# Optimization experiments

Measured on AMD Instinct MI355X. Metric: run time of the kernel, lower is better.

The kernel has to match this reference:

```python
import jax, jax.numpy as jnp
import numpy as np

N_SAMPLES = 2 ** 15  # 32768
NYQUIST = 22050.0 / 2.0
MIN_FREQ = 40.0 / NYQUIST
MAX_FREQ = 4000.0 / NYQUIST
FREQ_RANGE = MAX_FREQ - MIN_FREQ


def interp_linear(x, out_size):
    """torch F.interpolate(mode='linear', align_corners=False) along last axis."""
    in_size = x.shape[-1]
    scale = in_size / out_size
    coords = (jnp.arange(out_size, dtype=x.dtype) + 0.5) * scale - 0.5
    coords = jnp.clip(coords, 0.0, in_size - 1)
    lo = jnp.floor(coords).astype(jnp.int32)
    hi = jnp.minimum(lo + 1, in_size - 1)
    w = coords - lo.astype(x.dtype)
    return x[..., lo] * (1.0 - w) + x[..., hi] * w


def translate(pair, shift, scale):
    # angle of complex(pair[:,:,0], pair[:,:,1]) / pi, then affine
    angle = jnp.arctan2(pair[:, :, 1, :], pair[:, :, 0, :]) / np.pi
    return shift + angle * scale


def setup_inputs() -> dict:
    key = jax.random.key(0)
    k1, k2 = jax.random.split(key)
    x = jax.random.normal(k1, (16, 8, 10, 128), dtype=jnp.float32)
    noise = jax.random.normal(k2, (16, 8, N_SAMPLES), dtype=jnp.float32)
    return {"x": x, "noise": noise}


def reference(x, noise):
    # x: (batch, n_osc, 10, time_ctrl); noise: (batch, n_osc, N_SAMPLES)
    basic = x[:, :, 0:2, :]
    amp = jnp.sqrt(jnp.sum(basic * basic, axis=2))            # (b, o, t)
    amp = interp_linear(amp, N_SAMPLES)                       # (b, o, N)

    f0 = translate(basic, MIN_FREQ, FREQ_RANGE)               # control-rate
    mix = interp_linear(translate(x[:, :, 2:4, :], 1.0, 0.5), N_SAMPLES)
    harm_amp = amp * mix
    noise_amp = amp * (1.0 - mix)

    noise_std = translate(x[:, :, 4:6, :], MIN_FREQ, FREQ_RANGE)
    mod_factor = translate(x[:, :, 6:8, :], 0.25, 4.75)
    b = translate(x[:, :, 8:10, :], 0.1, 9.9)

    # band_filtered_noise: narrowband noise as a frequency-jittered sine
    f0_fr = interp_linear(f0, N_SAMPLES)
    std_fr = interp_linear(noise_std, N_SAMPLES)
    bfn = jnp.sin(jnp.cumsum(f0_fr + noise * std_fr, axis=-1))
    noise_sig = noise_amp * bfn

    mod_factor = interp_linear(mod_factor, N_SAMPLES)
    b = interp_linear(b, N_SAMPLES)
    mod = b * jnp.sin(jnp.cumsum(mod_factor, axis=-1))
    sig = harm_amp * jnp.sin(jnp.cumsum(f0_fr, axis=-1) + mod)

    mixed = noise_sig + sig                                   # (b, o, N)
    return jnp.mean(mixed, axis=1, keepdims=True)             # (b, 1, N)
```

## Files before the change

### kernel.cpp

```cpp
#include <hip/hip_runtime.h>
#include <math.h>

#define NS     32768
#define NB     128
#define CELL   32
#define CPB    32
#define PART   (CELL * CPB)
#define NPARTS (NS / PART)
#define TPB    256
#define NBATCH 16
#define GRID   (NBATCH * NPARTS)
#define NBIN   6

__device__ __forceinline__ float sinr(float x) {
    return __builtin_amdgcn_sinf(x - rintf(x));
}

__device__ __forceinline__ void seg_params(int i, int& lo, int& hi,
                                           double& w0, double& wst) {
    if (i < 128)            { lo = 0;   hi = 1;   w0 = 0.0; wst = 0.0; }
    else if (i >= NS - 128) { lo = 127; hi = 127; w0 = 0.0; wst = 0.0; }
    else {
        lo = (i - 128) >> 8;  hi = lo + 1;
        int off = (i - 128) & 255;
        w0 = (off + 0.5) * (1.0 / 256.0);
        wst = 1.0 / 256.0;
    }
}

__device__ __forceinline__ double bin_value(const float* xs, int q, int j) {
    const double PI_    = 3.14159265358979323846;
    const double INV2PI = 0.15915494309189533576888376337251;
    const double MINF   = 40.0 / 11025.0;
    const double FRNG   = (4000.0 - 40.0) / 11025.0;
    if (q == 0) {
        double a0 = (double)xs[j], a1 = (double)xs[NB + j];
        return sqrt(a0 * a0 + a1 * a1);
    }
    double ang = atan2((double)xs[(2 * q - 1) * NB + j],
                       (double)xs[(2 * q - 2) * NB + j]) / PI_;
    double sh, sc;
    if      (q == 1) { sh = MINF; sc = FRNG; }
    else if (q == 2) { sh = 1.0;  sc = 0.5;  }
    else if (q == 3) { sh = MINF; sc = FRNG; }
    else if (q == 4) { sh = 0.25; sc = 4.75; }
    else             { sh = 0.1;  sc = 9.9;  }
    double v = sh + ang * sc;
    if (q != 2) v *= INV2PI;
    return v;
}

__device__ __forceinline__ void cell_totals(
        const float4* nn, double f0L, double dF0, double stL, double dSt,
        double mfL, double dMf, double w0, double wst,
        double& t1, double& t3, double& t2) {
    float s0 = 0.f, s1 = 0.f;
    #pragma unroll
    for (int q4 = 0; q4 < CELL / 4; ++q4) {
        float4 nv = nn[q4];
        float jd = (float)(q4 * 4);
        s0 += nv.x; s1 = fmaf(jd, nv.x, s1);
        s0 += nv.y; s1 = fmaf(jd + 1.f, nv.y, s1);
        s0 += nv.z; s1 = fmaf(jd + 2.f, nv.z, s1);
        s0 += nv.w; s1 = fmaf(jd + 3.f, nv.w, s1);
    }
    double S0 = (double)s0, S1 = (double)s1;
    double sw = 32.0 * w0 + 496.0 * wst;
    t3 = 32.0 * f0L + dF0 * sw;
    t2 = 32.0 * mfL + dMf * sw;
    t1 = t3 + stL * S0 + dSt * (w0 * S0 + wst * S1);
}

__global__ __launch_bounds__(TPB)
void span_kernel(const float* __restrict__ xg, const float* __restrict__ ng,
                 double* __restrict__ wspan) {
    __shared__ double binsA[8][3][NBIN];

    int bx = blockIdx.x, bb = bx >> 5, p = bx & (NPARTS - 1);
    int tid = threadIdx.x, lane = tid & 63;
    int h = tid >> 5, c = tid & 31;
    int P = p * PART;
    int b0 = (P - 128) >> 8; if (b0 < 0) b0 = 0;
    int s  = (bb << 3) + h;
    int i0 = P + c * CELL;

    if (tid < 144) {
        int j = tid % NBIN, r = (tid / NBIN) % 3, h2 = tid / (3 * NBIN);
        int q = (r == 0) ? 1 : (r == 1) ? 3 : 4;
        const float* xs = xg + (size_t)((bb << 3) + h2) * 10 * NB;
        binsA[h2][r][j] = bin_value(xs, q, min(b0 + j, NB - 1));
    }
    __syncthreads();

    int lo, hi; double w0, wst;
    seg_params(i0, lo, hi, w0, wst);
    int jL = lo - b0, jH = hi - b0;
    double f0L = binsA[h][0][jL], dF0 = binsA[h][0][jH] - f0L;
    double stL = binsA[h][1][jL], dSt = binsA[h][1][jH] - stL;
    double mfL = binsA[h][2][jL], dMf = binsA[h][2][jH] - mfL;

    const float4* nn = reinterpret_cast<const float4*>(ng + (size_t)s * NS + i0);
    double t1, t3, t2;
    cell_totals(nn, f0L, dF0, stL, dSt, mfL, dMf, w0, wst, t1, t3, t2);

    double v1 = t1, v3 = t3, v2 = t2;
    #pragma unroll
    for (int d = 1; d < 32; d <<= 1) {
        double u1 = __shfl_up(v1, d);
        double u3 = __shfl_up(v3, d);
        double u2 = __shfl_up(v2, d);
        if ((lane & 31) >= d) { v1 += u1; v3 += u3; v2 += u2; }
    }
    if (c == 31) {
        size_t sb = ((size_t)s * NPARTS + p) * 3;
        wspan[sb + 0] = v1; wspan[sb + 1] = v3; wspan[sb + 2] = v2;
    }
}

__global__ __launch_bounds__(TPB)
void fm_kernel(const float* __restrict__ xg, const float* __restrict__ ng,
               const double* __restrict__ wspan, float* __restrict__ out) {
    __shared__ double binsA[8][3][NBIN];
    __shared__ float  binsB[8][6][NBIN];
    __shared__ double wtot[4][8][3];
    __shared__ double prefL[8][3];

    int bx = blockIdx.x, bb = bx >> 5, p = bx & (NPARTS - 1);
    int tid = threadIdx.x, lane = tid & 63, wid = tid >> 6;
    int h = tid & 7, c = tid >> 3;
    int P = p * PART;
    int b0 = (P - 128) >> 8; if (b0 < 0) b0 = 0;
    int s  = (bb << 3) + h;
    int i0 = P + c * CELL;

    if (tid < 192) {
        int r = tid & 7, g = tid >> 3, k = g % 3, h2 = g / 3;
        const double* sp = wspan + ((size_t)(((bb << 3) + h2) * NPARTS)) * 3 + k;
        double acc = 0.0;
        #pragma unroll
        for (int q = 0; q < NPARTS / 8; ++q) {
            int idx = r + q * 8;
            if (idx < p) acc += sp[idx * 3];
        }
        #pragma unroll
        for (int m = 1; m <= 4; m <<= 1) acc += __shfl_xor(acc, m);
        if (r == 0) prefL[h2][k] = acc;
    }
    for (int idx = tid; idx < 8 * 6 * NBIN; idx += TPB) {
        int j = idx % NBIN, q = (idx / NBIN) % 6, h2 = idx / (6 * NBIN);
        const float* xs = xg + (size_t)((bb << 3) + h2) * 10 * NB;
        double v = bin_value(xs, q, min(b0 + j, NB - 1));
        binsB[h2][q][j] = (float)v;
        if      (q == 1) binsA[h2][0][j] = v;
        else if (q == 3) binsA[h2][1][j] = v;
        else if (q == 4) binsA[h2][2][j] = v;
    }
    __syncthreads();

    int lo, hi; double w0, wst;
    seg_params(i0, lo, hi, w0, wst);
    int jL = lo - b0, jH = hi - b0;
    double f0L = binsA[h][0][jL], dF0 = binsA[h][0][jH] - f0L;
    double stL = binsA[h][1][jL], dSt = binsA[h][1][jH] - stL;
    double mfL = binsA[h][2][jL], dMf = binsA[h][2][jH] - mfL;

    const float4* nn = reinterpret_cast<const float4*>(ng + (size_t)s * NS + i0);
    double t1, t3, t2;
    cell_totals(nn, f0L, dF0, stL, dSt, mfL, dMf, w0, wst, t1, t3, t2);

    double v1 = t1, v3 = t3, v2 = t2;
    #pragma unroll
    for (int d = 8; d < 64; d <<= 1) {
        double u1 = __shfl_up(v1, d);
        double u3 = __shfl_up(v3, d);
        double u2 = __shfl_up(v2, d);
        if (lane >= d) { v1 += u1; v3 += u3; v2 += u2; }
    }
    if (lane >= 56) { wtot[wid][h][0] = v1; wtot[wid][h][1] = v3; wtot[wid][h][2] = v2; }
    __syncthreads();
    double b1 = 0.0, b3 = 0.0, b2 = 0.0;
    #pragma unroll
    for (int k = 0; k < 3; ++k)
        if (wid > k) { b1 += wtot[k][h][0]; b3 += wtot[k][h][1]; b2 += wtot[k][h][2]; }

    double a1 = prefL[h][0] + b1 + (v1 - t1);
    double a3 = prefL[h][1] + b3 + (v3 - t3);
    double a2 = prefL[h][2] + b2 + (v2 - t2);
    float fr1 = (float)(a1 - rint(a1));
    float fr3 = (float)(a3 - rint(a3));
    float fr2 = (float)(a2 - rint(a2));

    float amL = binsB[h][0][jL], dAm = binsB[h][0][jH] - amL;
    float g0L = binsB[h][1][jL], gF0 = binsB[h][1][jH] - g0L;
    float mxL = binsB[h][2][jL], dMx = binsB[h][2][jH] - mxL;
    float gsL = binsB[h][3][jL], gSt = binsB[h][3][jH] - gsL;
    float gmL = binsB[h][4][jL], gMf = binsB[h][4][jH] - gmL;
    float bbL = binsB[h][5][jL], dBb = binsB[h][5][jH] - bbL;
    float w0f = (float)w0, wsf = (float)wst;

    float arr[CELL];
    float d1 = 0.f, d2 = 0.f, d3 = 0.f;
    #pragma unroll
    for (int q4 = 0; q4 < CELL / 4; ++q4) {
        float4 nv = nn[q4];
        float nf[4] = {nv.x, nv.y, nv.z, nv.w};
        #pragma unroll
        for (int u = 0; u < 4; ++u) {
            int j = q4 * 4 + u;
            float wf  = fmaf((float)j, wsf, w0f);
            float f0v = fmaf(wf, gF0, g0L);
            float stv = fmaf(wf, gSt, gsL);
            float mfv = fmaf(wf, gMf, gmL);
            d3 += f0v;
            d1 += fmaf(nf[u], stv, f0v);
            d2 += mfv;
            float ampv = fmaf(wf, dAm, amL);
            float mixv = fmaf(wf, dMx, mxL);
            float bv   = fmaf(wf, dBb, bbL);
            float s2 = sinr(fr2 + d2);
            float s1 = sinr(fr1 + d1);
            float s3 = sinr(fmaf(bv, s2, fr3 + d3));
            float harm = ampv * mixv;
            arr[j] = fmaf(harm, s3, (ampv - harm) * s1);
        }
    }

    #pragma unroll
    for (int m = 1; m <= 4; m <<= 1) {
        #pragma unroll
        for (int j = 0; j < CELL; ++j) arr[j] += __shfl_xor(arr[j], m);
    }
    if (h == 0) {
        float4* op = reinterpret_cast<float4*>(out + (size_t)bb * NS + i0);
        #pragma unroll
        for (int j4 = 0; j4 < CELL / 4; ++j4)
            op[j4] = make_float4(arr[j4 * 4 + 0] * 0.125f, arr[j4 * 4 + 1] * 0.125f,
                                 arr[j4 * 4 + 2] * 0.125f, arr[j4 * 4 + 3] * 0.125f);
    }
}

extern "C" void kernel_launch(void* const* d_in, const int* in_sizes, int n_in,
                              void* d_out, int out_size, void* d_ws, size_t ws_size,
                              hipStream_t stream) {
    const float* x     = (const float*)d_in[0];
    const float* noise = (const float*)d_in[1];
    float* out = (float*)d_out;
    double* wspan = (double*)d_ws;
    span_kernel<<<GRID, TPB, 0, stream>>>(x, noise, wspan);
    fm_kernel<<<GRID, TPB, 0, stream>>>(x, noise, wspan, out);
}
```

Before: 79.56 us.

## Fuse span and FM kernels into one cooperative launch with grid sync

Merges the two-pass scan (span partial sums, then FM synthesis) into a single cooperative kernel that writes per-part totals, does a grid-wide sync, then reads the prefix. Noise values are kept in registers across the sync, so noise is read once instead of twice. This removes a kernel launch and the redundant bin and noise work of the first pass. The cost is a grid barrier, a requirement that all 512 blocks be co-resident (launch bounds set to 2 blocks per CU), and extra register pressure; it falls back to the two-kernel path if the cooperative launch fails.

Result: slower. 140.5 us (+76.6%).

```diff
diff --git a/kernel.cpp b/kernel.cpp
--- a/kernel.cpp
+++ b/kernel.cpp
@@ -1,5 +1,8 @@
 #include <hip/hip_runtime.h>
+#include <hip/hip_cooperative_groups.h>
 #include <math.h>
+
+namespace cg = cooperative_groups;
 
 #define NS     32768
 #define NB     128
@@ -51,8 +54,8 @@
 }
 
 __device__ __forceinline__ void cell_totals(
-        const float4* nn, double f0L, double dF0, double stL, double dSt,
-        double mfL, double dMf, double w0, double wst,
+        const float4 (&nn)[CELL / 4], double f0L, double dF0, double stL,
+        double dSt, double mfL, double dMf, double w0, double wst,
         double& t1, double& t3, double& t2) {
     float s0 = 0.f, s1 = 0.f;
     #pragma unroll
@@ -71,55 +74,9 @@
     t1 = t3 + stL * S0 + dSt * (w0 * S0 + wst * S1);
 }
 
-__global__ __launch_bounds__(TPB)
-void span_kernel(const float* __restrict__ xg, const float* __restrict__ ng,
-                 double* __restrict__ wspan) {
-    __shared__ double binsA[8][3][NBIN];
-
-    int bx = blockIdx.x, bb = bx >> 5, p = bx & (NPARTS - 1);
-    int tid = threadIdx.x, lane = tid & 63;
-    int h = tid >> 5, c = tid & 31;
-    int P = p * PART;
-    int b0 = (P - 128) >> 8; if (b0 < 0) b0 = 0;
-    int s  = (bb << 3) + h;
-    int i0 = P + c * CELL;
-
-    if (tid < 144) {
-        int j = tid % NBIN, r = (tid / NBIN) % 3, h2 = tid / (3 * NBIN);
-        int q = (r == 0) ? 1 : (r == 1) ? 3 : 4;
-        const float* xs = xg + (size_t)((bb << 3) + h2) * 10 * NB;
-        binsA[h2][r][j] = bin_value(xs, q, min(b0 + j, NB - 1));
-    }
-    __syncthreads();
-
-    int lo, hi; double w0, wst;
-    seg_params(i0, lo, hi, w0, wst);
-    int jL = lo - b0, jH = hi - b0;
-    double f0L = binsA[h][0][jL], dF0 = binsA[h][0][jH] - f0L;
-    double stL = binsA[h][1][jL], dSt = binsA[h][1][jH] - stL;
-    double mfL = binsA[h][2][jL], dMf = binsA[h][2][jH] - mfL;
-
-    const float4* nn = reinterpret_cast<const float4*>(ng + (size_t)s * NS + i0);
-    double t1, t3, t2;
-    cell_totals(nn, f0L, dF0, stL, dSt, mfL, dMf, w0, wst, t1, t3, t2);
-
-    double v1 = t1, v3 = t3, v2 = t2;
-    #pragma unroll
-    for (int d = 1; d < 32; d <<= 1) {
-        double u1 = __shfl_up(v1, d);
-        double u3 = __shfl_up(v3, d);
-        double u2 = __shfl_up(v2, d);
-        if ((lane & 31) >= d) { v1 += u1; v3 += u3; v2 += u2; }
-    }
-    if (c == 31) {
-        size_t sb = ((size_t)s * NPARTS + p) * 3;
-        wspan[sb + 0] = v1; wspan[sb + 1] = v3; wspan[sb + 2] = v2;
-    }
-}
-
-__global__ __launch_bounds__(TPB)
-void fm_kernel(const float* __restrict__ xg, const float* __restrict__ ng,
-               const double* __restrict__ wspan, float* __restrict__ out) {
+__global__ __launch_bounds__(TPB, 2)
+void fused_kernel(const float* __restrict__ xg, const float* __restrict__ ng,
+                  double* __restrict__ wspan, float* __restrict__ out) {
     __shared__ double binsA[8][3][NBIN];
     __shared__ float  binsB[8][6][NBIN];
     __shared__ double wtot[4][8][3];
@@ -133,19 +90,6 @@
     int s  = (bb << 3) + h;
     int i0 = P + c * CELL;
 
-    if (tid < 192) {
-        int r = tid & 7, g = tid >> 3, k = g % 3, h2 = g / 3;
-        const double* sp = wspan + ((size_t)(((bb << 3) + h2) * NPARTS)) * 3 + k;
-        double acc = 0.0;
-        #pragma unroll
-        for (int q = 0; q < NPARTS / 8; ++q) {
-            int idx = r + q * 8;
-            if (idx < p) acc += sp[idx * 3];
-        }
-        #pragma unroll
-        for (int m = 1; m <= 4; m <<= 1) acc += __shfl_xor(acc, m);
-        if (r == 0) prefL[h2][k] = acc;
-    }
     for (int idx = tid; idx < 8 * 6 * NBIN; idx += TPB) {
         int j = idx % NBIN, q = (idx / NBIN) % 6, h2 = idx / (6 * NBIN);
         const float* xs = xg + (size_t)((bb << 3) + h2) * 10 * NB;
@@ -160,13 +104,19 @@
     int lo, hi; double w0, wst;
     seg_params(i0, lo, hi, w0, wst);
     int jL = lo - b0, jH = hi - b0;
-    double f0L = binsA[h][0][jL], dF0 = binsA[h][0][jH] - f0L;
-    double stL = binsA[h][1][jL], dSt = binsA[h][1][jH] - stL;
-    double mfL = binsA[h][2][jL], dMf = binsA[h][2][jH] - mfL;
-
-    const float4* nn = reinterpret_cast<const float4*>(ng + (size_t)s * NS + i0);
+
+    const float4* np_ = reinterpret_cast<const float4*>(ng + (size_t)s * NS + i0);
+    float4 nv[CELL / 4];
+    #pragma unroll
+    for (int q4 = 0; q4 < CELL / 4; ++q4) nv[q4] = np_[q4];
+
     double t1, t3, t2;
-    cell_totals(nn, f0L, dF0, stL, dSt, mfL, dMf, w0, wst, t1, t3, t2);
+    {
+        double f0L = binsA[h][0][jL], dF0 = binsA[h][0][jH] - f0L;
+        double stL = binsA[h][1][jL], dSt = binsA[h][1][jH] - stL;
+        double mfL = binsA[h][2][jL], dMf = binsA[h][2][jH] - mfL;
+        cell_totals(nv, f0L, dF0, stL, dSt, mfL, dMf, w0, wst, t1, t3, t2);
+    }
 
     double v1 = t1, v3 = t3, v2 = t2;
     #pragma unroll
@@ -182,6 +132,28 @@
     #pragma unroll
     for (int k = 0; k < 3; ++k)
         if (wid > k) { b1 += wtot[k][h][0]; b3 += wtot[k][h][1]; b2 += wtot[k][h][2]; }
+
+    if (wid == 3 && lane >= 56) {
+        size_t sb = ((size_t)s * NPARTS + p) * 3;
+        wspan[sb + 0] = b1 + v1; wspan[sb + 1] = b3 + v3; wspan[sb + 2] = b2 + v2;
+    }
+
+    cg::this_grid().sync();
+
+    if (tid < 192) {
+        int r = tid & 7, g = tid >> 3, k = g % 3, h2 = g / 3;
+        const double* sp = wspan + ((size_t)(((bb << 3) + h2) * NPARTS)) * 3 + k;
+        double acc = 0.0;
+        #pragma unroll
+        for (int q = 0; q < NPARTS / 8; ++q) {
+            int idx = r + q * 8;
+            if (idx < p) acc += sp[idx * 3];
+        }
+        #pragma unroll
+        for (int m = 1; m <= 4; m <<= 1) acc += __shfl_xor(acc, m);
+        if (r == 0) prefL[h2][k] = acc;
+    }
+    __syncthreads();
 
     double a1 = prefL[h][0] + b1 + (v1 - t1);
     double a3 = prefL[h][1] + b3 + (v3 - t3);
@@ -202,8 +174,7 @@
     float d1 = 0.f, d2 = 0.f, d3 = 0.f;
     #pragma unroll
     for (int q4 = 0; q4 < CELL / 4; ++q4) {
-        float4 nv = nn[q4];
-        float nf[4] = {nv.x, nv.y, nv.z, nv.w};
+        float nf[4] = {nv[q4].x, nv[q4].y, nv[q4].z, nv[q4].w};
         #pragma unroll
         for (int u = 0; u < 4; ++u) {
             int j = q4 * 4 + u;
@@ -239,6 +210,179 @@
     }
 }
 
+__global__ __launch_bounds__(TPB)
+void span_kernel(const float* __restrict__ xg, const float* __restrict__ ng,
+                 double* __restrict__ wspan) {
+    __shared__ double binsA[8][3][NBIN];
+
+    int bx = blockIdx.x, bb = bx >> 5, p = bx & (NPARTS - 1);
+    int tid = threadIdx.x, lane = tid & 63;
+    int h = tid >> 5, c = tid & 31;
+    int P = p * PART;
+    int b0 = (P - 128) >> 8; if (b0 < 0) b0 = 0;
+    int s  = (bb << 3) + h;
+    int i0 = P + c * CELL;
+
+    if (tid < 144) {
+        int j = tid % NBIN, r = (tid / NBIN) % 3, h2 = tid / (3 * NBIN);
+        int q = (r == 0) ? 1 : (r == 1) ? 3 : 4;
+        const float* xs = xg + (size_t)((bb << 3) + h2) * 10 * NB;
+        binsA[h2][r][j] = bin_value(xs, q, min(b0 + j, NB - 1));
+    }
+    __syncthreads();
+
+    int lo, hi; double w0, wst;
+    seg_params(i0, lo, hi, w0, wst);
+    int jL = lo - b0, jH = hi - b0;
+    double f0L = binsA[h][0][jL], dF0 = binsA[h][0][jH] - f0L;
+    double stL = binsA[h][1][jL], dSt = binsA[h][1][jH] - stL;
+    double mfL = binsA[h][2][jL], dMf = binsA[h][2][jH] - mfL;
+
+    const float4* np_ = reinterpret_cast<const float4*>(ng + (size_t)s * NS + i0);
+    float4 nv[CELL / 4];
+    #pragma unroll
+    for (int q4 = 0; q4 < CELL / 4; ++q4) nv[q4] = np_[q4];
+    double t1, t3, t2;
+    cell_totals(nv, f0L, dF0, stL, dSt, mfL, dMf, w0, wst, t1, t3, t2);
+
+    double v1 = t1, v3 = t3, v2 = t2;
+    #pragma unroll
+    for (int d = 1; d < 32; d <<= 1) {
+        double u1 = __shfl_up(v1, d);
+        double u3 = __shfl_up(v3, d);
+        double u2 = __shfl_up(v2, d);
+        if ((lane & 31) >= d) { v1 += u1; v3 += u3; v2 += u2; }
+    }
+    if (c == 31) {
+        size_t sb = ((size_t)s * NPARTS + p) * 3;
+        wspan[sb + 0] = v1; wspan[sb + 1] = v3; wspan[sb + 2] = v2;
+    }
+}
+
+__global__ __launch_bounds__(TPB)
+void fm_kernel(const float* __restrict__ xg, const float* __restrict__ ng,
+               const double* __restrict__ wspan, float* __restrict__ out) {
+    __shared__ double binsA[8][3][NBIN];
+    __shared__ float  binsB[8][6][NBIN];
+    __shared__ double wtot[4][8][3];
+    __shared__ double prefL[8][3];
+
+    int bx = blockIdx.x, bb = bx >> 5, p = bx & (NPARTS - 1);
+    int tid = threadIdx.x, lane = tid & 63, wid = tid >> 6;
+    int h = tid & 7, c = tid >> 3;
+    int P = p * PART;
+    int b0 = (P - 128) >> 8; if (b0 < 0) b0 = 0;
+    int s  = (bb << 3) + h;
+    int i0 = P + c * CELL;
+
+    if (tid < 192) {
+        int r = tid & 7, g = tid >> 3, k = g % 3, h2 = g / 3;
+        const double* sp = wspan + ((size_t)(((bb << 3) + h2) * NPARTS)) * 3 + k;
+        double acc = 0.0;
+        #pragma unroll
+        for (int q = 0; q < NPARTS / 8; ++q) {
+            int idx = r + q * 8;
+            if (idx < p) acc += sp[idx * 3];
+        }
+        #pragma unroll
+        for (int m = 1; m <= 4; m <<= 1) acc += __shfl_xor(acc, m);
+        if (r == 0) prefL[h2][k] = acc;
+    }
+    for (int idx = tid; idx < 8 * 6 * NBIN; idx += TPB) {
+        int j = idx % NBIN, q = (idx / NBIN) % 6, h2 = idx / (6 * NBIN);
+        const float* xs = xg + (size_t)((bb << 3) + h2) * 10 * NB;
+        double v = bin_value(xs, q, min(b0 + j, NB - 1));
+        binsB[h2][q][j] = (float)v;
+        if      (q == 1) binsA[h2][0][j] = v;
+        else if (q == 3) binsA[h2][1][j] = v;
+        else if (q == 4) binsA[h2][2][j] = v;
+    }
+    __syncthreads();
+
+    int lo, hi; double w0, wst;
+    seg_params(i0, lo, hi, w0, wst);
+    int jL = lo - b0, jH = hi - b0;
+    double f0L = binsA[h][0][jL], dF0 = binsA[h][0][jH] - f0L;
+    double stL = binsA[h][1][jL], dSt = binsA[h][1][jH] - stL;
+    double mfL = binsA[h][2][jL], dMf = binsA[h][2][jH] - mfL;
+
+    const float4* np_ = reinterpret_cast<const float4*>(ng + (size_t)s * NS + i0);
+    float4 nv[CELL / 4];
+    #pragma unroll
+    for (int q4 = 0; q4 < CELL / 4; ++q4) nv[q4] = np_[q4];
+    double t1, t3, t2;
+    cell_totals(nv, f0L, dF0, stL, dSt, mfL, dMf, w0, wst, t1, t3, t2);
+
+    double v1 = t1, v3 = t3, v2 = t2;
+    #pragma unroll
+    for (int d = 8; d < 64; d <<= 1) {
+        double u1 = __shfl_up(v1, d);
+        double u3 = __shfl_up(v3, d);
+        double u2 = __shfl_up(v2, d);
+        if (lane >= d) { v1 += u1; v3 += u3; v2 += u2; }
+    }
+    if (lane >= 56) { wtot[wid][h][0] = v1; wtot[wid][h][1] = v3; wtot[wid][h][2] = v2; }
+    __syncthreads();
+    double b1 = 0.0, b3 = 0.0, b2 = 0.0;
+    #pragma unroll
+    for (int k = 0; k < 3; ++k)
+        if (wid > k) { b1 += wtot[k][h][0]; b3 += wtot[k][h][1]; b2 += wtot[k][h][2]; }
+
+    double a1 = prefL[h][0] + b1 + (v1 - t1);
+    double a3 = prefL[h][1] + b3 + (v3 - t3);
+    double a2 = prefL[h][2] + b2 + (v2 - t2);
+    float fr1 = (float)(a1 - rint(a1));
+    float fr3 = (float)(a3 - rint(a3));
+    float fr2 = (float)(a2 - rint(a2));
+
+    float amL = binsB[h][0][jL], dAm = binsB[h][0][jH] - amL;
+    float g0L = binsB[h][1][jL], gF0 = binsB[h][1][jH] - g0L;
+    float mxL = binsB[h][2][jL], dMx = binsB[h][2][jH] - mxL;
+    float gsL = binsB[h][3][jL], gSt = binsB[h][3][jH] - gsL;
+    float gmL = binsB[h][4][jL], gMf = binsB[h][4][jH] - gmL;
+    float bbL = binsB[h][5][jL], dBb = binsB[h][5][jH] - bbL;
+    float w0f = (float)w0, wsf = (float)wst;
+
+    float arr[CELL];
+    float d1 = 0.f, d2 = 0.f, d3 = 0.f;
+    #pragma unroll
+    for (int q4 = 0; q4 < CELL / 4; ++q4) {
+        float nf[4] = {nv[q4].x, nv[q4].y, nv[q4].z, nv[q4].w};
+        #pragma unroll
+        for (int u = 0; u < 4; ++u) {
+            int j = q4 * 4 + u;
+            float wf  = fmaf((float)j, wsf, w0f);
+            float f0v = fmaf(wf, gF0, g0L);
+            float stv = fmaf(wf, gSt, gsL);
+            float mfv = fmaf(wf, gMf, gmL);
+            d3 += f0v;
+            d1 += fmaf(nf[u], stv, f0v);
+            d2 += mfv;
+            float ampv = fmaf(wf, dAm, amL);
+            float mixv = fmaf(wf, dMx, mxL);
+            float bv   = fmaf(wf, dBb, bbL);
+            float s2 = sinr(fr2 + d2);
+            float s1 = sinr(fr1 + d1);
+            float s3 = sinr(fmaf(bv, s2, fr3 + d3));
+            float harm = ampv * mixv;
+            arr[j] = fmaf(harm, s3, (ampv - harm) * s1);
+        }
+    }
+
+    #pragma unroll
+    for (int m = 1; m <= 4; m <<= 1) {
+        #pragma unroll
+        for (int j = 0; j < CELL; ++j) arr[j] += __shfl_xor(arr[j], m);
+    }
+    if (h == 0) {
+        float4* op = reinterpret_cast<float4*>(out + (size_t)bb * NS + i0);
+        #pragma unroll
+        for (int j4 = 0; j4 < CELL / 4; ++j4)
+            op[j4] = make_float4(arr[j4 * 4 + 0] * 0.125f, arr[j4 * 4 + 1] * 0.125f,
+                                 arr[j4 * 4 + 2] * 0.125f, arr[j4 * 4 + 3] * 0.125f);
+    }
+}
+
 extern "C" void kernel_launch(void* const* d_in, const int* in_sizes, int n_in,
                               void* d_out, int out_size, void* d_ws, size_t ws_size,
                               hipStream_t stream) {
@@ -246,6 +390,12 @@
     const float* noise = (const float*)d_in[1];
     float* out = (float*)d_out;
     double* wspan = (double*)d_ws;
-    span_kernel<<<GRID, TPB, 0, stream>>>(x, noise, wspan);
-    fm_kernel<<<GRID, TPB, 0, stream>>>(x, noise, wspan, out);
-}
+    void* args[] = { (void*)&x, (void*)&noise, (void*)&wspan, (void*)&out };
+    hipError_t err = hipLaunchCooperativeKernel(
+        reinterpret_cast<void*>(fused_kernel), dim3(GRID), dim3(TPB),
+        args, 0, stream);
+    if (err != hipSuccess) {
+        span_kernel<<<GRID, TPB, 0, stream>>>(x, noise, wspan);
+        fm_kernel<<<GRID, TPB, 0, stream>>>(x, noise, wspan, out);
+    }
+}
```

## Shrink cells to 8 samples for 4x more blocks and prefetch noise

Applied to the files above, without the earlier changes.

Cuts the per-thread cell size from 32 to 8 samples, which gives 4x more partitions and blocks (NPARTS becomes 128) and reduces per-thread register and serial work. Noise float4 values are now loaded into registers at kernel start, before the bin setup and sync, so the load latency overlaps that work and the second read of the same data in fm_kernel goes away. The change also adds a launch_bounds occupancy hint and updates the bin counts and shift constants to match. The tradeoff is that the prefix of partition spans now sums over 128 entries per block, and the bin setup and scan overhead repeats across four times as many blocks.

Result: slower. 85.03 us (+6.9%).

```diff
diff --git a/kernel.cpp b/kernel.cpp
--- a/kernel.cpp
+++ b/kernel.cpp
@@ -3,14 +3,15 @@
 
 #define NS     32768
 #define NB     128
-#define CELL   32
+#define CELL   8
 #define CPB    32
 #define PART   (CELL * CPB)
 #define NPARTS (NS / PART)
 #define TPB    256
 #define NBATCH 16
 #define GRID   (NBATCH * NPARTS)
-#define NBIN   6
+#define NBIN   3
+#define SJ     ((CELL * (CELL - 1)) / 2)
 
 __device__ __forceinline__ float sinr(float x) {
     return __builtin_amdgcn_sinf(x - rintf(x));
@@ -51,8 +52,8 @@
 }
 
 __device__ __forceinline__ void cell_totals(
-        const float4* nn, double f0L, double dF0, double stL, double dSt,
-        double mfL, double dMf, double w0, double wst,
+        const float4 (&nn)[CELL / 4], double f0L, double dF0, double stL,
+        double dSt, double mfL, double dMf, double w0, double wst,
         double& t1, double& t3, double& t2) {
     float s0 = 0.f, s1 = 0.f;
     #pragma unroll
@@ -65,18 +66,18 @@
         s0 += nv.w; s1 = fmaf(jd + 3.f, nv.w, s1);
     }
     double S0 = (double)s0, S1 = (double)s1;
-    double sw = 32.0 * w0 + 496.0 * wst;
-    t3 = 32.0 * f0L + dF0 * sw;
-    t2 = 32.0 * mfL + dMf * sw;
+    double sw = (double)CELL * w0 + (double)SJ * wst;
+    t3 = (double)CELL * f0L + dF0 * sw;
+    t2 = (double)CELL * mfL + dMf * sw;
     t1 = t3 + stL * S0 + dSt * (w0 * S0 + wst * S1);
 }
 
-__global__ __launch_bounds__(TPB)
+__global__ __launch_bounds__(TPB, 4)
 void span_kernel(const float* __restrict__ xg, const float* __restrict__ ng,
                  double* __restrict__ wspan) {
     __shared__ double binsA[8][3][NBIN];
 
-    int bx = blockIdx.x, bb = bx >> 5, p = bx & (NPARTS - 1);
+    int bx = blockIdx.x, bb = bx >> 7, p = bx & (NPARTS - 1);
     int tid = threadIdx.x, lane = tid & 63;
     int h = tid >> 5, c = tid & 31;
     int P = p * PART;
@@ -84,7 +85,12 @@
     int s  = (bb << 3) + h;
     int i0 = P + c * CELL;
 
-    if (tid < 144) {
+    const float4* np_ = reinterpret_cast<const float4*>(ng + (size_t)s * NS + i0);
+    float4 nv[CELL / 4];
+    #pragma unroll
+    for (int q4 = 0; q4 < CELL / 4; ++q4) nv[q4] = np_[q4];
+
+    if (tid < 8 * 3 * NBIN) {
         int j = tid % NBIN, r = (tid / NBIN) % 3, h2 = tid / (3 * NBIN);
         int q = (r == 0) ? 1 : (r == 1) ? 3 : 4;
         const float* xs = xg + (size_t)((bb << 3) + h2) * 10 * NB;
@@ -99,9 +105,8 @@
     double stL = binsA[h][1][jL], dSt = binsA[h][1][jH] - stL;
     double mfL = binsA[h][2][jL], dMf = binsA[h][2][jH] - mfL;
 
-    const float4* nn = reinterpret_cast<const float4*>(ng + (size_t)s * NS + i0);
     double t1, t3, t2;
-    cell_totals(nn, f0L, dF0, stL, dSt, mfL, dMf, w0, wst, t1, t3, t2);
+    cell_totals(nv, f0L, dF0, stL, dSt, mfL, dMf, w0, wst, t1, t3, t2);
 
     double v1 = t1, v3 = t3, v2 = t2;
     #pragma unroll
@@ -117,7 +122,7 @@
     }
 }
 
-__global__ __launch_bounds__(TPB)
+__global__ __launch_bounds__(TPB, 4)
 void fm_kernel(const float* __restrict__ xg, const float* __restrict__ ng,
                const double* __restrict__ wspan, float* __restrict__ out) {
     __shared__ double binsA[8][3][NBIN];
@@ -125,7 +130,7 @@
     __shared__ double wtot[4][8][3];
     __shared__ double prefL[8][3];
 
-    int bx = blockIdx.x, bb = bx >> 5, p = bx & (NPARTS - 1);
+    int bx = blockIdx.x, bb = bx >> 7, p = bx & (NPARTS - 1);
     int tid = threadIdx.x, lane = tid & 63, wid = tid >> 6;
     int h = tid & 7, c = tid >> 3;
     int P = p * PART;
@@ -133,6 +138,11 @@
     int s  = (bb << 3) + h;
     int i0 = P + c * CELL;
 
+    const float4* np_ = reinterpret_cast<const float4*>(ng + (size_t)s * NS + i0);
+    float4 nv[CELL / 4];
+    #pragma unroll
+    for (int q4 = 0; q4 < CELL / 4; ++q4) nv[q4] = np_[q4];
+
     if (tid < 192) {
         int r = tid & 7, g = tid >> 3, k = g % 3, h2 = g / 3;
         const double* sp = wspan + ((size_t)(((bb << 3) + h2) * NPARTS)) * 3 + k;
@@ -146,8 +156,8 @@
         for (int m = 1; m <= 4; m <<= 1) acc += __shfl_xor(acc, m);
         if (r == 0) prefL[h2][k] = acc;
     }
-    for (int idx = tid; idx < 8 * 6 * NBIN; idx += TPB) {
-        int j = idx % NBIN, q = (idx / NBIN) % 6, h2 = idx / (6 * NBIN);
+    if (tid < 8 * 6 * NBIN) {
+        int j = tid % NBIN, q = (tid / NBIN) % 6, h2 = tid / (6 * NBIN);
         const float* xs = xg + (size_t)((bb << 3) + h2) * 10 * NB;
         double v = bin_value(xs, q, min(b0 + j, NB - 1));
         binsB[h2][q][j] = (float)v;
@@ -160,13 +170,14 @@
     int lo, hi; double w0, wst;
     seg_params(i0, lo, hi, w0, wst);
     int jL = lo - b0, jH = hi - b0;
-    double f0L = binsA[h][0][jL], dF0 = binsA[h][0][jH] - f0L;
-    double stL = binsA[h][1][jL], dSt = binsA[h][1][jH] - stL;
-    double mfL = binsA[h][2][jL], dMf = binsA[h][2][jH] - mfL;
-
-    const float4* nn = reinterpret_cast<const float4*>(ng + (size_t)s * NS + i0);
+
     double t1, t3, t2;
-    cell_totals(nn, f0L, dF0, stL, dSt, mfL, dMf, w0, wst, t1, t3, t2);
+    {
+        double f0L = binsA[h][0][jL], dF0 = binsA[h][0][jH] - f0L;
+        double stL = binsA[h][1][jL], dSt = binsA[h][1][jH] - stL;
+        double mfL = binsA[h][2][jL], dMf = binsA[h][2][jH] - mfL;
+        cell_totals(nv, f0L, dF0, stL, dSt, mfL, dMf, w0, wst, t1, t3, t2);
+    }
 
     double v1 = t1, v3 = t3, v2 = t2;
     #pragma unroll
@@ -202,8 +213,7 @@
     float d1 = 0.f, d2 = 0.f, d3 = 0.f;
     #pragma unroll
     for (int q4 = 0; q4 < CELL / 4; ++q4) {
-        float4 nv = nn[q4];
-        float nf[4] = {nv.x, nv.y, nv.z, nv.w};
+        float nf[4] = {nv[q4].x, nv[q4].y, nv[q4].z, nv[q4].w};
         #pragma unroll
         for (int u = 0; u < 4; ++u) {
             int j = q4 * 4 + u;
```
